# Kernel optimization log

Measured on AMD Instinct MI355X. Metric: run time of the kernel, lower is better.

The kernel has to match this reference:

```python
import jax, jax.numpy as jnp
import numpy as np

B, T, D_K, N_HEADS, D_FF, VOCAB, N_LAYERS = 4, 1024, 1024, 16, 4096, 65, 6


def setup_inputs() -> dict:
    key = jax.random.key(0)
    ks = jax.random.split(key, 12)
    f = lambda k, sh: jax.random.normal(k, sh, dtype=jnp.float32) * 0.02
    return {
        "batchData": jax.random.randint(ks[0], (B, T), 0, VOCAB),
        "target": jax.random.randint(ks[1], (B, T), 0, VOCAB),
        "pos": jnp.arange(T),
        "Wtok": f(ks[2], (VOCAB, D_K)),
        "Wpos": f(ks[3], (T, D_K)),
        "Wq": f(ks[4], (D_K, D_K)), "bq": jnp.zeros((D_K,), jnp.float32),
        "Wk": f(ks[5], (D_K, D_K)), "bk": jnp.zeros((D_K,), jnp.float32),
        "Wv": f(ks[6], (D_K, D_K)), "bv": jnp.zeros((D_K,), jnp.float32),
        "W1": f(ks[7], (D_K, D_FF)), "b1": jnp.zeros((D_FF,), jnp.float32),
        "W2": f(ks[8], (D_FF, D_K)), "b2": jnp.zeros((D_K,), jnp.float32),
        "ln_w": jnp.ones((D_K,), jnp.float32),
        "Wf": f(ks[9], (D_K, VOCAB)), "bf": jnp.zeros((VOCAB,), jnp.float32),
        "n_layers": N_LAYERS,
        "n_heads": N_HEADS,
    }


def layer_norm(x, w, eps=1e-5):
    m = jnp.mean(x, axis=-1, keepdims=True)
    v = jnp.var(x, axis=-1, keepdims=True)
    return (x - m) / jnp.sqrt(v + eps) * w


def reference(batchData, target, pos, Wtok, Wpos, Wq, bq, Wk, bk, Wv, bv,
              W1, b1, W2, b2, ln_w, Wf, bf, n_layers, n_heads):
    x = Wtok[batchData] + Wpos[pos]  # [B, T, C] (pos embedding broadcasts)
    Bsz, Tlen, C = x.shape
    dh = C // n_heads
    mask = jnp.tril(jnp.ones((Tlen, Tlen), dtype=bool))
    inv_sqrt_dk = 1.0 / jnp.sqrt(jnp.float32(C))  # source divides by sqrt(full d_k)

    def block(x):
        q = (x @ Wq + bq).reshape(Bsz, Tlen, n_heads, dh).transpose(0, 2, 1, 3)
        k = (x @ Wk + bk).reshape(Bsz, Tlen, n_heads, dh).transpose(0, 2, 1, 3)
        v = (x @ Wv + bv).reshape(Bsz, Tlen, n_heads, dh).transpose(0, 2, 1, 3)
        scores = jnp.einsum('bhqd,bhkd->bhqk', q, k) * inv_sqrt_dk
        scores = jnp.where(mask, scores, -jnp.inf)
        attn = jax.nn.softmax(scores, axis=-1)
        h = jnp.einsum('bhqk,bhkd->bhqd', attn, v)
        h = h.transpose(0, 2, 1, 3).reshape(Bsz, Tlen, C)
        h = h + layer_norm(h, ln_w)           # x = x + ln(x) (shared ln)
        ff = jax.nn.relu(h @ W1 + b1) @ W2 + b2
        return ff + layer_norm(ff, ln_w)      # same shared ln again

    # ModuleList repeats the SAME block object, so weights are shared across layers
    for _ in range(n_layers):
        x = block(x)

    logits = x @ Wf + bf                       # [B, T, V]
    probs = jax.nn.softmax(logits, axis=1)     # softmax over T, as in source
    pred = probs.reshape(Bsz * Tlen, -1)
    onehot = jax.nn.one_hot(target.reshape(-1), VOCAB, dtype=jnp.float32)
    # F.cross_entropy with soft (one-hot float) targets
    loss = -jnp.mean(jnp.sum(onehot * jax.nn.log_softmax(pred, axis=-1), axis=-1))
    return loss, probs
```

## Files before the change

### kernel.cpp

```cpp
#include <hip/hip_runtime.h>

typedef __attribute__((ext_vector_type(8))) short bh8;
typedef __attribute__((ext_vector_type(4))) float f4v;

constexpr int VOC = 65;
constexpr int NL  = 6;
constexpr int Mrow = 4096;

__device__ inline float b2f(unsigned short u) {
  union { unsigned int i; float f; } x; x.i = ((unsigned int)u) << 16; return x.f;
}
__device__ inline unsigned short f2b(float f) {
  union { float f; unsigned int i; } x; x.f = f;
  return (unsigned short)((x.i + 0x7FFFu + ((x.i >> 16) & 1u)) >> 16);
}
__device__ inline void gld16(const void* g, void* l) {
  __builtin_amdgcn_global_load_lds(
      (const __attribute__((address_space(1))) unsigned int*)g,
      (__attribute__((address_space(3))) unsigned int*)l, 16, 0, 0);
}
__device__ inline bh8 lds_swz(const unsigned short* base, int row, int colbyte) {
  int off = row * 128 + (colbyte ^ ((row & 7) << 4));
  return *(const bh8*)((const char*)base + off);
}
__device__ inline f4v mfma16(bh8 a, bh8 b, f4v c) {
  return __builtin_amdgcn_mfma_f32_16x16x32_bf16(a, b, c, 0, 0, 0);
}
#define VMCNT(n) asm volatile("s_waitcnt vmcnt(" #n ")" ::: "memory")

__global__ __launch_bounds__(256) void wt_conv(const float* __restrict__ src,
    unsigned short* __restrict__ dst, int K, int N) {
  __shared__ float t[32][33];
  int k0 = blockIdx.x * 32, n0 = blockIdx.y * 32;
  int tid = threadIdx.x;
#pragma unroll
  for (int i = 0; i < 4; ++i) {
    int idx = tid + i * 256;
    int kr = idx >> 5, nc = idx & 31;
    t[kr][nc] = (n0 + nc < N) ? src[(size_t)(k0 + kr) * N + n0 + nc] : 0.f;
  }
  __syncthreads();
#pragma unroll
  for (int i = 0; i < 4; ++i) {
    int idx = tid + i * 256;
    int nr = idx >> 5, kc = idx & 31;
    dst[(size_t)(n0 + nr) * K + k0 + kc] = f2b(t[kc][nr]);
  }
}

__global__ __launch_bounds__(256) void bias_prep(
    const float* __restrict__ bq, const float* __restrict__ bk,
    const float* __restrict__ bv, const float* __restrict__ bf,
    float* __restrict__ bqkv, float* __restrict__ bfp) {
  int i = blockIdx.x * 256 + threadIdx.x;
  if (i < 1024) bqkv[i] = bq[i];
  else if (i < 2048) bqkv[i] = bk[i - 1024];
  else if (i < 3072) bqkv[i] = bv[i - 2048];
  else if (i < 3200) bfp[i - 3072] = (i - 3072 < VOC) ? bf[i - 3072] : 0.f;
}

__global__ __launch_bounds__(256) void embed_bf(const int* __restrict__ tok,
    const float* __restrict__ Wtok, const float* __restrict__ Wpos,
    unsigned short* __restrict__ Xb) {
  int bt = blockIdx.x, t = bt & 1023, tid = threadIdx.x;
  int id = tok[bt];
  float4 a = ((const float4*)(Wtok + (size_t)id * 1024))[tid];
  float4 p = ((const float4*)(Wpos + (size_t)t * 1024))[tid];
  ushort4 o;
  o.x = f2b(a.x + p.x); o.y = f2b(a.y + p.y);
  o.z = f2b(a.z + p.z); o.w = f2b(a.w + p.w);
  ((ushort4*)(Xb + (size_t)bt * 1024))[tid] = o;
}

template <int TM, int TN, bool RELU, bool F32OUT, bool VT>
__global__ __launch_bounds__(256) void gemm_mfma(
    const unsigned short* __restrict__ A, const unsigned short* __restrict__ Bt,
    const float* __restrict__ bias, void* __restrict__ Cout,
    unsigned short* __restrict__ Vtout, long N, long K) {
  constexpr int MI = TM / 32, NI = TN / 32;
  constexpr int LNUM = MI + NI;
  constexpr int ABUF = TM * 64, BBUF = TN * 64;
  __shared__ unsigned short As[2 * ABUF];
  __shared__ unsigned short Bs[2 * BBUF];
  const int tid = threadIdx.x;
  const int lane = tid & 63, w = tid >> 6;
  const int wr = w >> 1, wc = w & 1;
  const int lr = lane & 15, lh = lane >> 4, lh4 = lh * 4;
  const long row0 = (long)blockIdx.x * TM, col0 = (long)blockIdx.y * TN;

  f4v acc[MI][NI];
#pragma unroll
  for (int i = 0; i < MI; ++i)
#pragma unroll
    for (int j = 0; j < NI; ++j) acc[i][j] = f4v{0.f, 0.f, 0.f, 0.f};

  const int rg = tid >> 3, s = tid & 7;
  const int ch = s ^ (rg & 7);
  const unsigned short* Ap = A + (row0 + rg) * K + ch * 8;
  const unsigned short* Bp = Bt + (col0 + rg) * K + ch * 8;

  auto stage = [&](int t, int buf) {
    const long k0 = (long)t << 6;
#pragma unroll
    for (int i = 0; i < MI; ++i)
      gld16(Ap + i * 32 * K + k0, &As[buf * ABUF + (i * 256 + tid) * 8]);
#pragma unroll
    for (int i = 0; i < NI; ++i)
      gld16(Bp + i * 32 * K + k0, &Bs[buf * BBUF + (i * 256 + tid) * 8]);
  };

  const int nt = (int)(K >> 6);
  stage(0, 0);

  for (int t = 0; t < nt; ++t) {
    const int cur = t & 1;
    if (t + 1 < nt) {
      stage(t + 1, cur ^ 1);
      if (LNUM == 8) { VMCNT(8); } else { VMCNT(6); }
    } else {
      VMCNT(0);
    }
    __builtin_amdgcn_s_barrier();
    const unsigned short* Ab = &As[cur * ABUF];
    const unsigned short* Bb = &Bs[cur * BBUF];
#pragma unroll
    for (int ks = 0; ks < 2; ++ks) {
      bh8 a[MI], b[NI];
      const int slot = ((ks << 2) | lh) ^ (lr & 7);
#pragma unroll
      for (int mi = 0; mi < MI; ++mi) {
        int m = wr * (TM / 2) + mi * 16 + lr;
        a[mi] = *(const bh8*)((const char*)Ab + m * 128 + slot * 16);
      }
#pragma unroll
      for (int ni = 0; ni < NI; ++ni) {
        int n = wc * (TN / 2) + ni * 16 + lr;
        b[ni] = *(const bh8*)((const char*)Bb + n * 128 + slot * 16);
      }
#pragma unroll
      for (int mi = 0; mi < MI; ++mi)
#pragma unroll
        for (int ni = 0; ni < NI; ++ni)
          acc[mi][ni] = mfma16(a[mi], b[ni], acc[mi][ni]);
    }
    __builtin_amdgcn_s_barrier();
  }

  if (VT && col0 >= 2048) {
#pragma unroll
    for (int mi = 0; mi < MI; ++mi) {
#pragma unroll
      for (int ni = 0; ni < NI; ++ni) {
        long col = col0 + wc * (TN / 2) + ni * 16 + lr;
        float bb = bias[col];
        int cc = (int)col - 2048;
        long row = row0 + wr * (TM / 2) + mi * 16 + lh4;
        int bi = (int)(row >> 10), tt = (int)(row & 1023);
        ushort4 o;
        o.x = f2b(acc[mi][ni][0] + bb);
        o.y = f2b(acc[mi][ni][1] + bb);
        o.z = f2b(acc[mi][ni][2] + bb);
        o.w = f2b(acc[mi][ni][3] + bb);
        *(ushort4*)&Vtout[((size_t)(bi * 16 + (cc >> 6)) * 64 + (cc & 63)) *
                              1024 + tt] = o;
      }
    }
    return;
  }
#pragma unroll
  for (int mi = 0; mi < MI; ++mi) {
#pragma unroll
    for (int ni = 0; ni < NI; ++ni) {
      long col = col0 + wc * (TN / 2) + ni * 16 + lr;
      float bb = bias[col];
#pragma unroll
      for (int r = 0; r < 4; ++r) {
        long row = row0 + wr * (TM / 2) + mi * 16 + lh4 + r;
        float v = acc[mi][ni][r] + bb;
        if (RELU) v = fmaxf(v, 0.f);
        if (F32OUT) ((float*)Cout)[row * N + col] = v;
        else ((unsigned short*)Cout)[row * N + col] = f2b(v);
      }
    }
  }
}

__global__ __launch_bounds__(256) void attn_mfma(
    const unsigned short* __restrict__ QKV, const unsigned short* __restrict__ Vt,
    unsigned short* __restrict__ Hout) {
  __shared__ unsigned short Ks[2][64 * 64];
  __shared__ unsigned short Vs[2][64 * 64];
  __shared__ unsigned short Ps[4][16 * 64];
  const int tid = threadIdx.x, w = tid >> 6, lane = tid & 63;
  const int qt = (int)gridDim.x - 1 - (int)blockIdx.x;
  const int bh = blockIdx.y;
  const int b = bh >> 4, h = bh & 15;
  const int lr = lane & 15, lh = lane >> 4, lh4 = lh * 4;

  const unsigned short* qp =
      QKV + (size_t)(b * 1024 + qt * 64 + w * 16 + lr) * 3072 + h * 64 + lh * 8;
  bh8 aq0 = *(const bh8*)qp;
  bh8 aq1 = *(const bh8*)(qp + 32);

  f4v o[4];
#pragma unroll
  for (int i = 0; i < 4; ++i) o[i] = f4v{0.f, 0.f, 0.f, 0.f};
  float m = -1e30f, l = 0.f;

  const int r8 = tid >> 3, slot = tid & 7;
  unsigned short* pw = &Ps[w][0];

  auto stage = [&](int kt, int buf) {
    int r = r8, c8 = (slot ^ (r & 7)) * 8;
    gld16(QKV + (size_t)(b * 1024 + kt * 64 + r) * 3072 + 1024 + h * 64 + c8,
          &Ks[buf][tid * 8]);
    gld16(Vt + (size_t)(bh * 64 + r) * 1024 + kt * 64 + c8, &Vs[buf][tid * 8]);
    r = r8 + 32; c8 = (slot ^ (r & 7)) * 8;
    gld16(QKV + (size_t)(b * 1024 + kt * 64 + r) * 3072 + 1024 + h * 64 + c8,
          &Ks[buf][2048 + tid * 8]);
    gld16(Vt + (size_t)(bh * 64 + r) * 1024 + kt * 64 + c8,
          &Vs[buf][2048 + tid * 8]);
  };

  stage(0, 0);

  for (int kt = 0; kt <= qt; ++kt) {
    const int cur = kt & 1;
    if (kt < qt) {
      stage(kt + 1, cur ^ 1);
      VMCNT(4);
    } else {
      VMCNT(0);
    }
    __builtin_amdgcn_s_barrier();

    f4v s[4];
#pragma unroll
    for (int nt = 0; nt < 4; ++nt) {
      bh8 k0 = lds_swz(Ks[cur], nt * 16 + lr, lh * 16);
      bh8 k1 = lds_swz(Ks[cur], nt * 16 + lr, lh * 16 + 64);
      f4v z = f4v{0.f, 0.f, 0.f, 0.f};
      z = mfma16(k0, aq0, z);
      z = mfma16(k1, aq1, z);
      s[nt] = z;
    }
    const bool diag = (kt == qt);
    const int qloc = w * 16 + lr;
#pragma unroll
    for (int nt = 0; nt < 4; ++nt)
#pragma unroll
      for (int r = 0; r < 4; ++r) {
        float v = s[nt][r] * 0.03125f;
        if (diag && (nt * 16 + lh4 + r) > qloc) v = -1e30f;
        s[nt][r] = v;
      }
    float tm = s[0][0];
#pragma unroll
    for (int nt = 0; nt < 4; ++nt)
#pragma unroll
      for (int r = 0; r < 4; ++r) tm = fmaxf(tm, s[nt][r]);
    tm = fmaxf(tm, __shfl_xor(tm, 16));
    tm = fmaxf(tm, __shfl_xor(tm, 32));
    float mn = fmaxf(m, tm);
    float corr = __expf(m - mn);
    m = mn;
    float sum = 0.f;
#pragma unroll
    for (int nt = 0; nt < 4; ++nt)
#pragma unroll
      for (int r = 0; r < 4; ++r) {
        float e = __expf(s[nt][r] - mn);
        s[nt][r] = e;
        sum += e;
      }
    sum += __shfl_xor(sum, 16);
    sum += __shfl_xor(sum, 32);
    l = l * corr + sum;
#pragma unroll
    for (int nt = 0; nt < 4; ++nt) {
      unsigned int u0, u1;
      asm("v_cvt_pk_bf16_f32 %0, %1, %2" : "=v"(u0) : "v"(s[nt][0]), "v"(s[nt][1]));
      asm("v_cvt_pk_bf16_f32 %0, %1, %2" : "=v"(u1) : "v"(s[nt][2]), "v"(s[nt][3]));
      uint2 pk{u0, u1};
      *(uint2*)((char*)pw + lr * 128 + ((nt * 32 + lh * 8) ^ ((lr & 7) << 4))) = pk;
    }
    float c0 = __shfl(corr, lh4 + 0), c1 = __shfl(corr, lh4 + 1);
    float c2 = __shfl(corr, lh4 + 2), c3 = __shfl(corr, lh4 + 3);
#pragma unroll
    for (int nt = 0; nt < 4; ++nt) {
      o[nt][0] *= c0; o[nt][1] *= c1; o[nt][2] *= c2; o[nt][3] *= c3;
    }
    bh8 pa0 = lds_swz(pw, lr, lh * 16);
    bh8 pa1 = lds_swz(pw, lr, lh * 16 + 64);
#pragma unroll
    for (int nt = 0; nt < 4; ++nt) {
      bh8 v0 = lds_swz(Vs[cur], nt * 16 + lr, lh * 16);
      bh8 v1 = lds_swz(Vs[cur], nt * 16 + lr, lh * 16 + 64);
      o[nt] = mfma16(pa0, v0, o[nt]);
      o[nt] = mfma16(pa1, v1, o[nt]);
    }
    __builtin_amdgcn_s_barrier();
  }
  float linv = 1.f / l;
  float l0 = __shfl(linv, lh4 + 0), l1 = __shfl(linv, lh4 + 1);
  float l2 = __shfl(linv, lh4 + 2), l3 = __shfl(linv, lh4 + 3);
  const size_t rowb = (size_t)(b * 1024 + qt * 64 + w * 16);
#pragma unroll
  for (int nt = 0; nt < 4; ++nt) {
    int col = h * 64 + nt * 16 + lr;
    Hout[(rowb + lh4 + 0) * 1024 + col] = f2b(o[nt][0] * l0);
    Hout[(rowb + lh4 + 1) * 1024 + col] = f2b(o[nt][1] * l1);
    Hout[(rowb + lh4 + 2) * 1024 + col] = f2b(o[nt][2] * l2);
    Hout[(rowb + lh4 + 3) * 1024 + col] = f2b(o[nt][3] * l3);
  }
}

__global__ __launch_bounds__(256) void ln_res_bf(
    const unsigned short* __restrict__ Xi, const float* __restrict__ wln,
    unsigned short* __restrict__ Y) {
  int row = blockIdx.x, tid = threadIdx.x;
  ushort4 u = ((const ushort4*)(Xi + (size_t)row * 1024))[tid];
  float x0 = b2f(u.x), x1 = b2f(u.y), x2 = b2f(u.z), x3 = b2f(u.w);
  float s = x0 + x1 + x2 + x3;
  float ss = x0 * x0 + x1 * x1 + x2 * x2 + x3 * x3;
#pragma unroll
  for (int off = 32; off; off >>= 1) {
    s += __shfl_xor(s, off);
    ss += __shfl_xor(ss, off);
  }
  __shared__ float sw[4], ssw[4];
  int wv = tid >> 6, ln = tid & 63;
  if (ln == 0) { sw[wv] = s; ssw[wv] = ss; }
  __syncthreads();
  s = sw[0] + sw[1] + sw[2] + sw[3];
  ss = ssw[0] + ssw[1] + ssw[2] + ssw[3];
  float mean = s * (1.f / 1024.f);
  float var = ss * (1.f / 1024.f) - mean * mean;
  float rstd = rsqrtf(var + 1e-5f);
  float4 wv4 = ((const float4*)wln)[tid];
  ushort4 out;
  out.x = f2b(x0 + (x0 - mean) * rstd * wv4.x);
  out.y = f2b(x1 + (x1 - mean) * rstd * wv4.y);
  out.z = f2b(x2 + (x2 - mean) * rstd * wv4.z);
  out.w = f2b(x3 + (x3 - mean) * rstd * wv4.w);
  ((ushort4*)(Y + (size_t)row * 1024))[tid] = out;
}

__global__ __launch_bounds__(256) void softmaxT_kernel(
    const float* __restrict__ logits, float* __restrict__ probs) {
  int b = blockIdx.x / VOC;
  int v = blockIdx.x - b * VOC;
  const float* src = logits + (size_t)b * 1024 * 128 + v;
  float vals[4];
  float m = -1e30f;
#pragma unroll
  for (int i = 0; i < 4; ++i) {
    int t = threadIdx.x + 256 * i;
    vals[i] = src[(size_t)t * 128];
    m = fmaxf(m, vals[i]);
  }
#pragma unroll
  for (int off = 32; off; off >>= 1) m = fmaxf(m, __shfl_xor(m, off));
  __shared__ float sm[4], ssum[4];
  int wv = threadIdx.x >> 6, ln = threadIdx.x & 63;
  if (ln == 0) sm[wv] = m;
  __syncthreads();
  m = fmaxf(fmaxf(sm[0], sm[1]), fmaxf(sm[2], sm[3]));
  float s = 0.f;
#pragma unroll
  for (int i = 0; i < 4; ++i) { vals[i] = __expf(vals[i] - m); s += vals[i]; }
#pragma unroll
  for (int off = 32; off; off >>= 1) s += __shfl_xor(s, off);
  if (ln == 0) ssum[wv] = s;
  __syncthreads();
  s = ssum[0] + ssum[1] + ssum[2] + ssum[3];
  float inv = 1.f / s;
  float* dst = probs + (size_t)b * 1024 * VOC + v;
#pragma unroll
  for (int i = 0; i < 4; ++i) {
    int t = threadIdx.x + 256 * i;
    dst[(size_t)t * VOC] = vals[i] * inv;
  }
}

__global__ __launch_bounds__(256) void loss_rows_kernel(
    const float* __restrict__ probs, const int* __restrict__ tgt,
    float* __restrict__ partial) {
  int wv = threadIdx.x >> 6, lane = threadIdx.x & 63;
  int row = blockIdx.x * 4 + wv;
  const float* p = probs + (size_t)row * VOC;
  float x0 = p[lane];
  float x1 = (lane == 0) ? p[64] : -1e30f;
  float m = fmaxf(x0, x1);
#pragma unroll
  for (int off = 32; off; off >>= 1) m = fmaxf(m, __shfl_xor(m, off));
  float s = __expf(x0 - m) + ((lane == 0) ? __expf(x1 - m) : 0.f);
#pragma unroll
  for (int off = 32; off; off >>= 1) s += __shfl_xor(s, off);
  if (lane == 0) {
    int tg = tgt[row];
    partial[row] = (p[tg] - m) - logf(s);
  }
}

__global__ __launch_bounds__(256) void loss_final_kernel(
    const float* __restrict__ partial, float* __restrict__ out) {
  float s = 0.f;
  for (int i = threadIdx.x; i < Mrow; i += 256) s += partial[i];
#pragma unroll
  for (int off = 32; off; off >>= 1) s += __shfl_xor(s, off);
  __shared__ float sw[4];
  int wv = threadIdx.x >> 6, ln = threadIdx.x & 63;
  if (ln == 0) sw[wv] = s;
  __syncthreads();
  if (threadIdx.x == 0) out[0] = -(sw[0] + sw[1] + sw[2] + sw[3]) / (float)Mrow;
}

extern "C" void kernel_launch(void* const* d_in, const int* in_sizes, int n_in,
                              void* d_out, int out_size, void* d_ws,
                              size_t ws_size, hipStream_t stream) {
  (void)in_sizes; (void)n_in; (void)out_size; (void)ws_size;
  const int*   tok    = (const int*)d_in[0];
  const int*   target = (const int*)d_in[1];
  const float* Wtok   = (const float*)d_in[3];
  const float* Wpos   = (const float*)d_in[4];
  const float* Wq = (const float*)d_in[5];  const float* bq = (const float*)d_in[6];
  const float* Wk = (const float*)d_in[7];  const float* bk = (const float*)d_in[8];
  const float* Wv = (const float*)d_in[9];  const float* bv = (const float*)d_in[10];
  const float* W1 = (const float*)d_in[11]; const float* b1 = (const float*)d_in[12];
  const float* W2 = (const float*)d_in[13]; const float* b2 = (const float*)d_in[14];
  const float* lnw = (const float*)d_in[15];
  const float* Wf = (const float*)d_in[16]; const float* bf = (const float*)d_in[17];
  float* out = (float*)d_out;

  char* p = (char*)d_ws;
  unsigned short* Xb    = (unsigned short*)p; p += (size_t)Mrow * 1024 * 2;
  unsigned short* QKVb  = (unsigned short*)p; p += (size_t)Mrow * 3072 * 2;
  unsigned short* Vt    = (unsigned short*)p; p += (size_t)64 * 64 * 1024 * 2;
  unsigned short* Hb    = (unsigned short*)p; p += (size_t)Mrow * 1024 * 2;
  unsigned short* F2b   = (unsigned short*)p; p += (size_t)Mrow * 1024 * 2;
  unsigned short* FF1b  = (unsigned short*)p; p += (size_t)Mrow * 4096 * 2;
  unsigned short* WqkvT = (unsigned short*)p; p += (size_t)3072 * 1024 * 2;
  unsigned short* W1T   = (unsigned short*)p; p += (size_t)4096 * 1024 * 2;
  unsigned short* W2T   = (unsigned short*)p; p += (size_t)1024 * 4096 * 2;
  unsigned short* WfT   = (unsigned short*)p; p += (size_t)128 * 1024 * 2;
  float* bqkv = (float*)p; p += 3072 * 4;
  float* bfp  = (float*)p; p += 128 * 4;
  float* LOG  = (float*)p; p += (size_t)Mrow * 128 * 4;
  float* PART = (float*)p; p += Mrow * 4;

  wt_conv<<<dim3(32, 32), 256, 0, stream>>>(Wq, WqkvT,                1024, 1024);
  wt_conv<<<dim3(32, 32), 256, 0, stream>>>(Wk, WqkvT + 1024 * 1024,  1024, 1024);
  wt_conv<<<dim3(32, 32), 256, 0, stream>>>(Wv, WqkvT + 2048 * 1024,  1024, 1024);
  wt_conv<<<dim3(32, 128), 256, 0, stream>>>(W1, W1T, 1024, 4096);
  wt_conv<<<dim3(128, 32), 256, 0, stream>>>(W2, W2T, 4096, 1024);
  wt_conv<<<dim3(32, 4), 256, 0, stream>>>(Wf, WfT, 1024, VOC);
  bias_prep<<<13, 256, 0, stream>>>(bq, bk, bv, bf, bqkv, bfp);

  embed_bf<<<Mrow, 256, 0, stream>>>(tok, Wtok, Wpos, Xb);

  for (int l = 0; l < NL; ++l) {
    gemm_mfma<64, 128, false, false, true><<<dim3(64, 24), 256, 0, stream>>>(
        Xb, WqkvT, bqkv, QKVb, Vt, 3072, 1024);
    attn_mfma<<<dim3(16, 64), 256, 0, stream>>>(QKVb, Vt, Hb);
    ln_res_bf<<<Mrow, 256, 0, stream>>>(Hb, lnw, F2b);
    gemm_mfma<128, 128, true, false, false><<<dim3(32, 32), 256, 0, stream>>>(
        F2b, W1T, b1, FF1b, nullptr, 4096, 1024);
    gemm_mfma<64, 128, false, false, false><<<dim3(64, 8), 256, 0, stream>>>(
        FF1b, W2T, b2, Hb, nullptr, 1024, 4096);
    ln_res_bf<<<Mrow, 256, 0, stream>>>(Hb, lnw, Xb);
  }

  gemm_mfma<64, 128, false, true, false><<<dim3(64, 1), 256, 0, stream>>>(
      Xb, WfT, bfp, LOG, nullptr, 128, 1024);
  softmaxT_kernel<<<4 * VOC, 256, 0, stream>>>(LOG, out + 1);
  loss_rows_kernel<<<Mrow / 4, 256, 0, stream>>>(out + 1, target, PART);
  loss_final_kernel<<<1, 256, 0, stream>>>(PART, out);
}
```

Before: 1.104 ms.

## Switch GEMM to 32x32x16 MFMA and enlarge QKV/W2 tiles to 128x128

Rewrites the GEMM inner loop to issue 32x32x16 bf16 MFMAs instead of 16x16x32 ones. All four k-slices of LDS fragments are loaded first, then the MFMAs run back to back, with the epilogue index mapping updated to match. The QKV and W2 GEMMs move from 64x128 to 128x128 tiles. The aim is more math per LDS read and better operand reuse. The cost is higher register pressure and fewer blocks: the W2 GEMM now launches only 256 blocks.

```diff
diff --git a/kernel.cpp b/kernel.cpp
--- a/kernel.cpp
+++ b/kernel.cpp
@@ -2,6 +2,7 @@
 
 typedef __attribute__((ext_vector_type(8))) short bh8;
 typedef __attribute__((ext_vector_type(4))) float f4v;
+typedef __attribute__((ext_vector_type(16))) float f16a;
 
 constexpr int VOC = 65;
 constexpr int NL  = 6;
@@ -25,6 +26,9 @@
 }
 __device__ inline f4v mfma16(bh8 a, bh8 b, f4v c) {
   return __builtin_amdgcn_mfma_f32_16x16x32_bf16(a, b, c, 0, 0, 0);
+}
+__device__ inline f16a mfma32(bh8 a, bh8 b, f16a c) {
+  return __builtin_amdgcn_mfma_f32_32x32x16_bf16(a, b, c, 0, 0, 0);
 }
 #define VMCNT(n) asm volatile("s_waitcnt vmcnt(" #n ")" ::: "memory")
 
@@ -77,22 +81,25 @@
     const unsigned short* __restrict__ A, const unsigned short* __restrict__ Bt,
     const float* __restrict__ bias, void* __restrict__ Cout,
     unsigned short* __restrict__ Vtout, long N, long K) {
-  constexpr int MI = TM / 32, NI = TN / 32;
-  constexpr int LNUM = MI + NI;
+  constexpr int MI = TM / 64, NI = TN / 64;
+  constexpr int AL = TM / 32, BL = TN / 32;
+  constexpr int LNUM = AL + BL;
   constexpr int ABUF = TM * 64, BBUF = TN * 64;
   __shared__ unsigned short As[2 * ABUF];
   __shared__ unsigned short Bs[2 * BBUF];
   const int tid = threadIdx.x;
   const int lane = tid & 63, w = tid >> 6;
   const int wr = w >> 1, wc = w & 1;
-  const int lr = lane & 15, lh = lane >> 4, lh4 = lh * 4;
+  const int l31 = lane & 31, l5 = lane >> 5;
   const long row0 = (long)blockIdx.x * TM, col0 = (long)blockIdx.y * TN;
 
-  f4v acc[MI][NI];
+  f16a acc[MI][NI];
 #pragma unroll
   for (int i = 0; i < MI; ++i)
 #pragma unroll
-    for (int j = 0; j < NI; ++j) acc[i][j] = f4v{0.f, 0.f, 0.f, 0.f};
+    for (int j = 0; j < NI; ++j)
+#pragma unroll
+      for (int r = 0; r < 16; ++r) acc[i][j][r] = 0.f;
 
   const int rg = tid >> 3, s = tid & 7;
   const int ch = s ^ (rg & 7);
@@ -102,10 +109,10 @@
   auto stage = [&](int t, int buf) {
     const long k0 = (long)t << 6;
 #pragma unroll
-    for (int i = 0; i < MI; ++i)
+    for (int i = 0; i < AL; ++i)
       gld16(Ap + i * 32 * K + k0, &As[buf * ABUF + (i * 256 + tid) * 8]);
 #pragma unroll
-    for (int i = 0; i < NI; ++i)
+    for (int i = 0; i < BL; ++i)
       gld16(Bp + i * 32 * K + k0, &Bs[buf * BBUF + (i * 256 + tid) * 8]);
   };
 
@@ -123,26 +130,28 @@
     __builtin_amdgcn_s_barrier();
     const unsigned short* Ab = &As[cur * ABUF];
     const unsigned short* Bb = &Bs[cur * BBUF];
-#pragma unroll
-    for (int ks = 0; ks < 2; ++ks) {
-      bh8 a[MI], b[NI];
-      const int slot = ((ks << 2) | lh) ^ (lr & 7);
+    bh8 a[MI][4], b[NI][4];
+#pragma unroll
+    for (int ks = 0; ks < 4; ++ks) {
+      const int slot = (ks * 2 + l5) ^ (l31 & 7);
 #pragma unroll
       for (int mi = 0; mi < MI; ++mi) {
-        int m = wr * (TM / 2) + mi * 16 + lr;
-        a[mi] = *(const bh8*)((const char*)Ab + m * 128 + slot * 16);
+        int m = wr * (TM / 2) + mi * 32 + l31;
+        a[mi][ks] = *(const bh8*)((const char*)Ab + m * 128 + slot * 16);
       }
 #pragma unroll
       for (int ni = 0; ni < NI; ++ni) {
-        int n = wc * (TN / 2) + ni * 16 + lr;
-        b[ni] = *(const bh8*)((const char*)Bb + n * 128 + slot * 16);
+        int n = wc * (TN / 2) + ni * 32 + l31;
+        b[ni][ks] = *(const bh8*)((const char*)Bb + n * 128 + slot * 16);
       }
+    }
+#pragma unroll
+    for (int ks = 0; ks < 4; ++ks)
 #pragma unroll
       for (int mi = 0; mi < MI; ++mi)
 #pragma unroll
         for (int ni = 0; ni < NI; ++ni)
-          acc[mi][ni] = mfma16(a[mi], b[ni], acc[mi][ni]);
-    }
+          acc[mi][ni] = mfma32(a[mi][ks], b[ni][ks], acc[mi][ni]);
     __builtin_amdgcn_s_barrier();
   }
 
@@ -151,18 +160,21 @@
     for (int mi = 0; mi < MI; ++mi) {
 #pragma unroll
       for (int ni = 0; ni < NI; ++ni) {
-        long col = col0 + wc * (TN / 2) + ni * 16 + lr;
+        int col = (int)col0 + wc * (TN / 2) + ni * 32 + l31;
         float bb = bias[col];
-        int cc = (int)col - 2048;
-        long row = row0 + wr * (TM / 2) + mi * 16 + lh4;
-        int bi = (int)(row >> 10), tt = (int)(row & 1023);
-        ushort4 o;
-        o.x = f2b(acc[mi][ni][0] + bb);
-        o.y = f2b(acc[mi][ni][1] + bb);
-        o.z = f2b(acc[mi][ni][2] + bb);
-        o.w = f2b(acc[mi][ni][3] + bb);
-        *(ushort4*)&Vtout[((size_t)(bi * 16 + (cc >> 6)) * 64 + (cc & 63)) *
-                              1024 + tt] = o;
+        int cc = col - 2048;
+#pragma unroll
+        for (int q = 0; q < 4; ++q) {
+          long row = row0 + wr * (TM / 2) + mi * 32 + q * 8 + l5 * 4;
+          int bi = (int)(row >> 10), tt = (int)(row & 1023);
+          ushort4 o;
+          o.x = f2b(acc[mi][ni][q * 4 + 0] + bb);
+          o.y = f2b(acc[mi][ni][q * 4 + 1] + bb);
+          o.z = f2b(acc[mi][ni][q * 4 + 2] + bb);
+          o.w = f2b(acc[mi][ni][q * 4 + 3] + bb);
+          *(ushort4*)&Vtout[((size_t)(bi * 16 + (cc >> 6)) * 64 + (cc & 63)) *
+                                1024 + tt] = o;
+        }
       }
     }
     return;
@@ -171,16 +183,18 @@
   for (int mi = 0; mi < MI; ++mi) {
 #pragma unroll
     for (int ni = 0; ni < NI; ++ni) {
-      long col = col0 + wc * (TN / 2) + ni * 16 + lr;
+      long col = col0 + wc * (TN / 2) + ni * 32 + l31;
       float bb = bias[col];
 #pragma unroll
-      for (int r = 0; r < 4; ++r) {
-        long row = row0 + wr * (TM / 2) + mi * 16 + lh4 + r;
-        float v = acc[mi][ni][r] + bb;
-        if (RELU) v = fmaxf(v, 0.f);
-        if (F32OUT) ((float*)Cout)[row * N + col] = v;
-        else ((unsigned short*)Cout)[row * N + col] = f2b(v);
-      }
+      for (int q = 0; q < 4; ++q)
+#pragma unroll
+        for (int j = 0; j < 4; ++j) {
+          long row = row0 + wr * (TM / 2) + mi * 32 + q * 8 + l5 * 4 + j;
+          float v = acc[mi][ni][q * 4 + j] + bb;
+          if (RELU) v = fmaxf(v, 0.f);
+          if (F32OUT) ((float*)Cout)[row * N + col] = v;
+          else ((unsigned short*)Cout)[row * N + col] = f2b(v);
+        }
     }
   }
 }
@@ -460,13 +474,13 @@
   embed_bf<<<Mrow, 256, 0, stream>>>(tok, Wtok, Wpos, Xb);
 
   for (int l = 0; l < NL; ++l) {
-    gemm_mfma<64, 128, false, false, true><<<dim3(64, 24), 256, 0, stream>>>(
+    gemm_mfma<128, 128, false, false, true><<<dim3(32, 24), 256, 0, stream>>>(
         Xb, WqkvT, bqkv, QKVb, Vt, 3072, 1024);
     attn_mfma<<<dim3(16, 64), 256, 0, stream>>>(QKVb, Vt, Hb);
     ln_res_bf<<<Mrow, 256, 0, stream>>>(Hb, lnw, F2b);
     gemm_mfma<128, 128, true, false, false><<<dim3(32, 32), 256, 0, stream>>>(
         F2b, W1T, b1, FF1b, nullptr, 4096, 1024);
-    gemm_mfma<64, 128, false, false, false><<<dim3(64, 8), 256, 0, stream>>>(
+    gemm_mfma<128, 128, false, false, false><<<dim3(32, 8), 256, 0, stream>>>(
         FF1b, W2T, b2, Hb, nullptr, 1024, 4096);
     ln_res_bf<<<Mrow, 256, 0, stream>>>(Hb, lnw, Xb);
   }
```

Measured after the change: 1.237 ms. 12.0% more time.

## Add 512-thread 256x128 triple-buffered GEMM with split-K FF2 and fused reduce-LN

Applied to the files above, without the earlier changes.

Adds a new gemm8 kernel with 256x128 tiles and 8 waves. It uses a 32-wide K step, a three-stage global_load_lds pipeline, an XCD-aware block remap and s_setprio around the MFMA block. QKV, FF1 and FF2 now use it. FF2 is split four ways along K into bf16 partial planes that reuse the QKV/Vt buffer, and a new ln2_fuse kernel sums the partials, adds b2 and applies the residual layer norm. The aim is more data reuse per tile, better latency hiding and more blocks for the narrow FF2 GEMM. In exchange it adds partial-sum traffic and rounds each partial to bf16 before the sum.

```diff
diff --git a/kernel.cpp b/kernel.cpp
--- a/kernel.cpp
+++ b/kernel.cpp
@@ -26,7 +26,8 @@
 __device__ inline f4v mfma16(bh8 a, bh8 b, f4v c) {
   return __builtin_amdgcn_mfma_f32_16x16x32_bf16(a, b, c, 0, 0, 0);
 }
-#define VMCNT(n) asm volatile("s_waitcnt vmcnt(" #n ")" ::: "memory")
+#define WAITV(n) asm volatile("s_waitcnt vmcnt(" #n ")" ::: "memory")
+#define WAITVL(n) asm volatile("s_waitcnt vmcnt(" #n ") lgkmcnt(0)" ::: "memory")
 
 __global__ __launch_bounds__(256) void wt_conv(const float* __restrict__ src,
     unsigned short* __restrict__ dst, int K, int N) {
@@ -72,13 +73,133 @@
   ((ushort4*)(Xb + (size_t)bt * 1024))[tid] = o;
 }
 
-template <int TM, int TN, bool RELU, bool F32OUT, bool VT>
-__global__ __launch_bounds__(256) void gemm_mfma(
+template <bool RELU, bool PART, bool VT>
+__global__ __launch_bounds__(512) void gemm8(
     const unsigned short* __restrict__ A, const unsigned short* __restrict__ Bt,
     const float* __restrict__ bias, void* __restrict__ Cout,
-    unsigned short* __restrict__ Vtout, long N, long K) {
+    unsigned short* __restrict__ Vtout, long N, long Kloop, long lda, long ldb,
+    int MT, int NT) {
+  __shared__ unsigned short As[3 * 256 * 32];
+  __shared__ unsigned short Bs[3 * 128 * 32];
+  const int tid = threadIdx.x;
+  const int lane = tid & 63, w = tid >> 6;
+  const int wr = w >> 1, wc = w & 1;
+  const int lr = lane & 15, lh = lane >> 4, lh4 = lh * 4;
+
+  const int nwg = (int)gridDim.x;
+  const int wid = ((int)blockIdx.x & 7) * (nwg >> 3) + ((int)blockIdx.x >> 3);
+  const int rowT = wid % MT, rest = wid / MT;
+  const int colT = rest % NT, ksl = rest / NT;
+  const long row0 = (long)rowT * 256, col0 = (long)colT * 128;
+  const long kOff = (long)ksl * Kloop;
+
+  f4v acc[4][4];
+#pragma unroll
+  for (int i = 0; i < 4; ++i)
+#pragma unroll
+    for (int j = 0; j < 4; ++j) acc[i][j] = f4v{0.f, 0.f, 0.f, 0.f};
+
+  const int rg = tid >> 2, s = tid & 3;
+  const int ch = s ^ ((rg ^ (rg >> 2)) & 3);
+  const unsigned short* ApA0 = A + (row0 + rg) * lda + kOff + ch * 8;
+  const unsigned short* ApA1 = ApA0 + 128 * lda;
+  const unsigned short* BpB  = Bt + (col0 + rg) * ldb + kOff + ch * 8;
+
+  auto stage = [&](int t, int buf) {
+    const long k0 = (long)t << 5;
+    gld16(ApA0 + k0, &As[buf * 8192 + tid * 8]);
+    gld16(ApA1 + k0, &As[buf * 8192 + 4096 + tid * 8]);
+    gld16(BpB  + k0, &Bs[buf * 4096 + tid * 8]);
+  };
+
+  const int nt = (int)(Kloop >> 5);
+  stage(0, 0);
+  stage(1, 1);
+
+  const int fl = (lr ^ (lr >> 2)) & 3;
+  const int slot = lh ^ fl;
+
+  for (int t = 0; t < nt; ++t) {
+    if (t + 1 < nt) { WAITVL(3); } else { WAITVL(0); }
+    __builtin_amdgcn_s_barrier();
+    __builtin_amdgcn_sched_barrier(0);
+    const unsigned short* Ab = &As[(t % 3) * 8192];
+    const unsigned short* Bb = &Bs[(t % 3) * 4096];
+    bh8 a[4], b[4];
+#pragma unroll
+    for (int mi = 0; mi < 4; ++mi)
+      a[mi] = *(const bh8*)&Ab[(wr * 64 + mi * 16 + lr) * 32 + slot * 8];
+#pragma unroll
+    for (int ni = 0; ni < 4; ++ni)
+      b[ni] = *(const bh8*)&Bb[(wc * 64 + ni * 16 + lr) * 32 + slot * 8];
+    if (t + 2 < nt) stage(t + 2, (t + 2) % 3);
+    __builtin_amdgcn_s_setprio(1);
+#pragma unroll
+    for (int mi = 0; mi < 4; ++mi)
+#pragma unroll
+      for (int ni = 0; ni < 4; ++ni)
+        acc[mi][ni] = mfma16(a[mi], b[ni], acc[mi][ni]);
+    __builtin_amdgcn_s_setprio(0);
+  }
+
+  if (PART) {
+    unsigned short* P = (unsigned short*)Cout + (size_t)ksl * 4096 * 1024;
+#pragma unroll
+    for (int mi = 0; mi < 4; ++mi)
+#pragma unroll
+      for (int ni = 0; ni < 4; ++ni) {
+        long col = col0 + wc * 64 + ni * 16 + lr;
+#pragma unroll
+        for (int r = 0; r < 4; ++r) {
+          long row = row0 + wr * 64 + mi * 16 + lh4 + r;
+          P[row * N + col] = f2b(acc[mi][ni][r]);
+        }
+      }
+    return;
+  }
+  if (VT && col0 >= 2048) {
+#pragma unroll
+    for (int mi = 0; mi < 4; ++mi) {
+#pragma unroll
+      for (int ni = 0; ni < 4; ++ni) {
+        int col = (int)col0 + wc * 64 + ni * 16 + lr;
+        float bb = bias[col];
+        int cc = col - 2048;
+        long row = row0 + wr * 64 + mi * 16 + lh4;
+        int bi = (int)(row >> 10), tt = (int)(row & 1023);
+        ushort4 o;
+        o.x = f2b(acc[mi][ni][0] + bb);
+        o.y = f2b(acc[mi][ni][1] + bb);
+        o.z = f2b(acc[mi][ni][2] + bb);
+        o.w = f2b(acc[mi][ni][3] + bb);
+        *(ushort4*)&Vtout[((size_t)(bi * 16 + (cc >> 6)) * 64 + (cc & 63)) *
+                              1024 + tt] = o;
+      }
+    }
+    return;
+  }
+#pragma unroll
+  for (int mi = 0; mi < 4; ++mi) {
+#pragma unroll
+    for (int ni = 0; ni < 4; ++ni) {
+      long col = col0 + wc * 64 + ni * 16 + lr;
+      float bb = bias[col];
+#pragma unroll
+      for (int r = 0; r < 4; ++r) {
+        long row = row0 + wr * 64 + mi * 16 + lh4 + r;
+        float v = acc[mi][ni][r] + bb;
+        if (RELU) v = fmaxf(v, 0.f);
+        ((unsigned short*)Cout)[row * N + col] = f2b(v);
+      }
+    }
+  }
+}
+
+template <int TM, int TN, bool RELU, bool F32OUT>
+__global__ __launch_bounds__(256) void gemm4(
+    const unsigned short* __restrict__ A, const unsigned short* __restrict__ Bt,
+    const float* __restrict__ bias, void* __restrict__ Cout, long N, long K) {
   constexpr int MI = TM / 32, NI = TN / 32;
-  constexpr int LNUM = MI + NI;
   constexpr int ABUF = TM * 64, BBUF = TN * 64;
   __shared__ unsigned short As[2 * ABUF];
   __shared__ unsigned short Bs[2 * BBUF];
@@ -87,18 +208,15 @@
   const int wr = w >> 1, wc = w & 1;
   const int lr = lane & 15, lh = lane >> 4, lh4 = lh * 4;
   const long row0 = (long)blockIdx.x * TM, col0 = (long)blockIdx.y * TN;
-
   f4v acc[MI][NI];
 #pragma unroll
   for (int i = 0; i < MI; ++i)
 #pragma unroll
     for (int j = 0; j < NI; ++j) acc[i][j] = f4v{0.f, 0.f, 0.f, 0.f};
-
   const int rg = tid >> 3, s = tid & 7;
   const int ch = s ^ (rg & 7);
   const unsigned short* Ap = A + (row0 + rg) * K + ch * 8;
   const unsigned short* Bp = Bt + (col0 + rg) * K + ch * 8;
-
   auto stage = [&](int t, int buf) {
     const long k0 = (long)t << 6;
 #pragma unroll
@@ -108,17 +226,15 @@
     for (int i = 0; i < NI; ++i)
       gld16(Bp + i * 32 * K + k0, &Bs[buf * BBUF + (i * 256 + tid) * 8]);
   };
-
   const int nt = (int)(K >> 6);
   stage(0, 0);
-
   for (int t = 0; t < nt; ++t) {
     const int cur = t & 1;
     if (t + 1 < nt) {
       stage(t + 1, cur ^ 1);
-      if (LNUM == 8) { VMCNT(8); } else { VMCNT(6); }
+      WAITV(6);
     } else {
-      VMCNT(0);
+      WAITV(0);
     }
     __builtin_amdgcn_s_barrier();
     const unsigned short* Ab = &As[cur * ABUF];
@@ -144,28 +260,6 @@
           acc[mi][ni] = mfma16(a[mi], b[ni], acc[mi][ni]);
     }
     __builtin_amdgcn_s_barrier();
-  }
-
-  if (VT && col0 >= 2048) {
-#pragma unroll
-    for (int mi = 0; mi < MI; ++mi) {
-#pragma unroll
-      for (int ni = 0; ni < NI; ++ni) {
-        long col = col0 + wc * (TN / 2) + ni * 16 + lr;
-        float bb = bias[col];
-        int cc = (int)col - 2048;
-        long row = row0 + wr * (TM / 2) + mi * 16 + lh4;
-        int bi = (int)(row >> 10), tt = (int)(row & 1023);
-        ushort4 o;
-        o.x = f2b(acc[mi][ni][0] + bb);
-        o.y = f2b(acc[mi][ni][1] + bb);
-        o.z = f2b(acc[mi][ni][2] + bb);
-        o.w = f2b(acc[mi][ni][3] + bb);
-        *(ushort4*)&Vtout[((size_t)(bi * 16 + (cc >> 6)) * 64 + (cc & 63)) *
-                              1024 + tt] = o;
-      }
-    }
-    return;
   }
 #pragma unroll
   for (int mi = 0; mi < MI; ++mi) {
@@ -228,9 +322,9 @@
     const int cur = kt & 1;
     if (kt < qt) {
       stage(kt + 1, cur ^ 1);
-      VMCNT(4);
+      WAITV(4);
     } else {
-      VMCNT(0);
+      WAITV(0);
     }
     __builtin_amdgcn_s_barrier();
 
@@ -346,6 +440,44 @@
   ((ushort4*)(Y + (size_t)row * 1024))[tid] = out;
 }
 
+__global__ __launch_bounds__(256) void ln2_fuse(
+    const unsigned short* __restrict__ P, const float* __restrict__ b2,
+    const float* __restrict__ wln, unsigned short* __restrict__ Y) {
+  int row = blockIdx.x, tid = threadIdx.x;
+  const size_t plane = (size_t)4096 * 1024;
+  float x0 = 0.f, x1 = 0.f, x2 = 0.f, x3 = 0.f;
+#pragma unroll
+  for (int pl = 0; pl < 4; ++pl) {
+    ushort4 u = *(const ushort4*)&P[pl * plane + (size_t)row * 1024 + tid * 4];
+    x0 += b2f(u.x); x1 += b2f(u.y); x2 += b2f(u.z); x3 += b2f(u.w);
+  }
+  float4 bb = ((const float4*)b2)[tid];
+  x0 += bb.x; x1 += bb.y; x2 += bb.z; x3 += bb.w;
+  float s = x0 + x1 + x2 + x3;
+  float ss = x0 * x0 + x1 * x1 + x2 * x2 + x3 * x3;
+#pragma unroll
+  for (int off = 32; off; off >>= 1) {
+    s += __shfl_xor(s, off);
+    ss += __shfl_xor(ss, off);
+  }
+  __shared__ float sw[4], ssw[4];
+  int wv = tid >> 6, ln = tid & 63;
+  if (ln == 0) { sw[wv] = s; ssw[wv] = ss; }
+  __syncthreads();
+  s = sw[0] + sw[1] + sw[2] + sw[3];
+  ss = ssw[0] + ssw[1] + ssw[2] + ssw[3];
+  float mean = s * (1.f / 1024.f);
+  float var = ss * (1.f / 1024.f) - mean * mean;
+  float rstd = rsqrtf(var + 1e-5f);
+  float4 wv4 = ((const float4*)wln)[tid];
+  ushort4 out;
+  out.x = f2b(x0 + (x0 - mean) * rstd * wv4.x);
+  out.y = f2b(x1 + (x1 - mean) * rstd * wv4.y);
+  out.z = f2b(x2 + (x2 - mean) * rstd * wv4.z);
+  out.w = f2b(x3 + (x3 - mean) * rstd * wv4.w);
+  ((ushort4*)(Y + (size_t)row * 1024))[tid] = out;
+}
+
 __global__ __launch_bounds__(256) void softmaxT_kernel(
     const float* __restrict__ logits, float* __restrict__ probs) {
   int b = blockIdx.x / VOC;
@@ -448,6 +580,7 @@
   float* bfp  = (float*)p; p += 128 * 4;
   float* LOG  = (float*)p; p += (size_t)Mrow * 128 * 4;
   float* PART = (float*)p; p += Mrow * 4;
+  unsigned short* Pff2 = QKVb;
 
   wt_conv<<<dim3(32, 32), 256, 0, stream>>>(Wq, WqkvT,                1024, 1024);
   wt_conv<<<dim3(32, 32), 256, 0, stream>>>(Wk, WqkvT + 1024 * 1024,  1024, 1024);
@@ -460,19 +593,19 @@
   embed_bf<<<Mrow, 256, 0, stream>>>(tok, Wtok, Wpos, Xb);
 
   for (int l = 0; l < NL; ++l) {
-    gemm_mfma<64, 128, false, false, true><<<dim3(64, 24), 256, 0, stream>>>(
-        Xb, WqkvT, bqkv, QKVb, Vt, 3072, 1024);
+    gemm8<false, false, true><<<384, 512, 0, stream>>>(
+        Xb, WqkvT, bqkv, QKVb, Vt, 3072, 1024, 1024, 1024, 16, 24);
     attn_mfma<<<dim3(16, 64), 256, 0, stream>>>(QKVb, Vt, Hb);
     ln_res_bf<<<Mrow, 256, 0, stream>>>(Hb, lnw, F2b);
-    gemm_mfma<128, 128, true, false, false><<<dim3(32, 32), 256, 0, stream>>>(
-        F2b, W1T, b1, FF1b, nullptr, 4096, 1024);
-    gemm_mfma<64, 128, false, false, false><<<dim3(64, 8), 256, 0, stream>>>(
-        FF1b, W2T, b2, Hb, nullptr, 1024, 4096);
-    ln_res_bf<<<Mrow, 256, 0, stream>>>(Hb, lnw, Xb);
-  }
-
-  gemm_mfma<64, 128, false, true, false><<<dim3(64, 1), 256, 0, stream>>>(
-      Xb, WfT, bfp, LOG, nullptr, 128, 1024);
+    gemm8<true, false, false><<<512, 512, 0, stream>>>(
+        F2b, W1T, b1, FF1b, nullptr, 4096, 1024, 1024, 1024, 16, 32);
+    gemm8<false, true, false><<<512, 512, 0, stream>>>(
+        FF1b, W2T, nullptr, Pff2, nullptr, 1024, 1024, 4096, 4096, 16, 8);
+    ln2_fuse<<<Mrow, 256, 0, stream>>>(Pff2, b2, lnw, Xb);
+  }
+
+  gemm4<64, 128, false, true><<<dim3(64, 1), 256, 0, stream>>>(
+      Xb, WfT, bfp, LOG, 128, 1024);
   softmaxT_kernel<<<4 * VOC, 256, 0, stream>>>(LOG, out + 1);
   loss_rows_kernel<<<Mrow / 4, 256, 0, stream>>>(out + 1, target, PART);
   loss_final_kernel<<<1, 256, 0, stream>>>(PART, out);
```

Measured after the change: 1.048 ms. -5.1%, faster.
